# Optimization experiments

Hardware: AMD Instinct MI355X
Metric: run time of the kernel (lower is better)

Reference implementation:

```python
import jax, jax.numpy as jnp
import numpy as np

D = 1024
H = 16
HD = D // H
N_TEXT = 256
N_VISION = 256
N_FRAMES = 12


def setup_inputs() -> dict:
    key = jax.random.key(0)
    ks = jax.random.split(key, 10)
    s = 1.0 / np.sqrt(D)
    return {
        "text_hidden_states": jax.random.normal(ks[0], (N_TEXT, D), jnp.float32),
        "vision_hidden_states": jax.random.normal(ks[1], (N_VISION, N_FRAMES, D), jnp.float32),
        "wq": jax.random.normal(ks[2], (D, D), jnp.float32) * s,
        "bq": jnp.zeros((D,), jnp.float32),
        "wk": jax.random.normal(ks[3], (D, D), jnp.float32) * s,
        "bk": jnp.zeros((D,), jnp.float32),
        "wv": jax.random.normal(ks[4], (D, D), jnp.float32) * s,
        "bv": jnp.zeros((D,), jnp.float32),
        "wo": jax.random.normal(ks[5], (D, D), jnp.float32) * s,
        "bo": jnp.zeros((D,), jnp.float32),
    }


def reference(text_hidden_states, vision_hidden_states, wq, bq, wk, bk, wv, bv, wo, bo):
    n_text = text_hidden_states.shape[0]
    n_vision, n_frames, _ = vision_hidden_states.shape
    # projections (torch Linear: x @ W.T + b)
    q = (text_hidden_states @ wq.T + bq).reshape(n_text, H, HD)            # [t,h,d]
    k = (vision_hidden_states @ wk.T + bk).reshape(n_vision, n_frames, H, HD)  # [v,f,h,d]
    v = (vision_hidden_states @ wv.T + bv).reshape(n_vision, n_frames, H, HD)  # [v,f,h,d]
    # shared query broadcast over vision batch: scores [v,h,f,t]
    scores = jnp.einsum("vfhd,thd->vhft", k, q) / jnp.sqrt(jnp.asarray(HD, scores_dtype := q.dtype))
    probs = jax.nn.softmax(scores, axis=2)  # softmax over frames (dim=2)
    # attn_output [v,t,h,d] -> [v,t,D]
    out = jnp.einsum("vfhd,vhft->vthd", v, probs).reshape(n_vision, n_text, D)
    return out @ wo.T + bo
```

## Files before the change

### kernel.cpp

```cpp
#include <hip/hip_runtime.h>

typedef short bf16x8 __attribute__((ext_vector_type(8)));
typedef float f32x4 __attribute__((ext_vector_type(4)));

__device__ __forceinline__ unsigned short f2bf(float f) {
  union { float f; unsigned u; } x; x.f = f;
  unsigned u = x.u;
  u += 0x7fffu + ((u >> 16) & 1u);
  return (unsigned short)(u >> 16);
}

__global__ __launch_bounds__(256) void cvt_all(
    const float* __restrict__ text, const float* __restrict__ vis,
    const float* __restrict__ wq, const float* __restrict__ wk,
    const float* __restrict__ wv, const float* __restrict__ wo,
    unsigned short* __restrict__ o0, unsigned short* __restrict__ o1,
    unsigned short* __restrict__ o2, unsigned short* __restrict__ o3,
    unsigned short* __restrict__ o4, unsigned short* __restrict__ o5)
{
  long i4 = (long)blockIdx.x * 256 + threadIdx.x;
  const float* src; unsigned short* dst; long base;
  if      (i4 <   65536) { src = text; dst = o0; base = 0; }
  else if (i4 <  851968) { src = vis;  dst = o1; base = 65536; }
  else if (i4 < 1114112) { src = wq;   dst = o2; base = 851968; }
  else if (i4 < 1376256) { src = wk;   dst = o3; base = 1114112; }
  else if (i4 < 1638400) { src = wv;   dst = o4; base = 1376256; }
  else                   { src = wo;   dst = o5; base = 1638400; }
  long li = i4 - base;
  float4 f = reinterpret_cast<const float4*>(src)[li];
  uint2 u;
  u.x = (unsigned)f2bf(f.x) | ((unsigned)f2bf(f.y) << 16);
  u.y = (unsigned)f2bf(f.z) | ((unsigned)f2bf(f.w) << 16);
  reinterpret_cast<uint2*>(dst)[li] = u;
}

__global__ __launch_bounds__(256) void gemm_abt_bf16(
    const unsigned short* __restrict__ A,
    const unsigned short* __restrict__ B,
    unsigned short* __restrict__ C,
    const float* __restrict__ bias,
    int K, int lda, int ldb, int ldc)
{
  __shared__ unsigned short As[64][40];
  __shared__ unsigned short Bs[64][40];
  const int m0 = blockIdx.y * 64, n0 = blockIdx.x * 64;
  const int tid = threadIdx.x;
  const int lane = tid & 63, w = tid >> 6;
  const int wm = w >> 1, wn = w & 1;
  const int r16 = lane & 15, kg = lane >> 4;
  const int srow = tid >> 2, sseg = tid & 3;

  const f32x4 fzero = {0.f, 0.f, 0.f, 0.f};
  f32x4 acc[2][2];
#pragma unroll
  for (int i = 0; i < 2; ++i)
#pragma unroll
    for (int j = 0; j < 2; ++j) acc[i][j] = fzero;

  for (int k0 = 0; k0 < K; k0 += 32) {
    __syncthreads();
    *reinterpret_cast<int4*>(&As[srow][sseg * 8]) =
        *reinterpret_cast<const int4*>(&A[(long)(m0 + srow) * lda + k0 + sseg * 8]);
    *reinterpret_cast<int4*>(&Bs[srow][sseg * 8]) =
        *reinterpret_cast<const int4*>(&B[(long)(n0 + srow) * ldb + k0 + sseg * 8]);
    __syncthreads();
    bf16x8 a[2], b[2];
#pragma unroll
    for (int i = 0; i < 2; ++i)
      a[i] = *reinterpret_cast<const bf16x8*>(&As[wm * 32 + i * 16 + r16][kg * 8]);
#pragma unroll
    for (int j = 0; j < 2; ++j)
      b[j] = *reinterpret_cast<const bf16x8*>(&Bs[wn * 32 + j * 16 + r16][kg * 8]);
#pragma unroll
    for (int i = 0; i < 2; ++i)
#pragma unroll
      for (int j = 0; j < 2; ++j)
        acc[i][j] = __builtin_amdgcn_mfma_f32_16x16x32_bf16(a[i], b[j], acc[i][j], 0, 0, 0);
  }
#pragma unroll
  for (int i = 0; i < 2; ++i) {
#pragma unroll
    for (int j = 0; j < 2; ++j) {
      const int row = m0 + wm * 32 + i * 16 + kg * 4;
      const int col = n0 + wn * 32 + j * 16 + r16;
      const float bv = bias ? bias[col] : 0.f;
#pragma unroll
      for (int r = 0; r < 4; ++r)
        C[(long)(row + r) * ldc + col] = f2bf(acc[i][j][r] + bv);
    }
  }
}

__global__ __launch_bounds__(256) void gemm_abt_bf16_kv(
    const unsigned short* __restrict__ A,
    const unsigned short* __restrict__ B0,
    const unsigned short* __restrict__ B1,
    unsigned short* __restrict__ C0,
    unsigned short* __restrict__ C1,
    const float* __restrict__ bias0,
    const float* __restrict__ bias1,
    int K, int lda, int ldb, int ldc)
{
  const unsigned short* B = blockIdx.z ? B1 : B0;
  unsigned short* C = blockIdx.z ? C1 : C0;
  const float* bias = blockIdx.z ? bias1 : bias0;

  __shared__ unsigned short As[64][40];
  __shared__ unsigned short Bs[64][40];
  const int m0 = blockIdx.y * 64, n0 = blockIdx.x * 64;
  const int tid = threadIdx.x;
  const int lane = tid & 63, w = tid >> 6;
  const int wm = w >> 1, wn = w & 1;
  const int r16 = lane & 15, kg = lane >> 4;
  const int srow = tid >> 2, sseg = tid & 3;

  const f32x4 fzero = {0.f, 0.f, 0.f, 0.f};
  f32x4 acc[2][2];
#pragma unroll
  for (int i = 0; i < 2; ++i)
#pragma unroll
    for (int j = 0; j < 2; ++j) acc[i][j] = fzero;

  for (int k0 = 0; k0 < K; k0 += 32) {
    __syncthreads();
    *reinterpret_cast<int4*>(&As[srow][sseg * 8]) =
        *reinterpret_cast<const int4*>(&A[(long)(m0 + srow) * lda + k0 + sseg * 8]);
    *reinterpret_cast<int4*>(&Bs[srow][sseg * 8]) =
        *reinterpret_cast<const int4*>(&B[(long)(n0 + srow) * ldb + k0 + sseg * 8]);
    __syncthreads();
    bf16x8 a[2], b[2];
#pragma unroll
    for (int i = 0; i < 2; ++i)
      a[i] = *reinterpret_cast<const bf16x8*>(&As[wm * 32 + i * 16 + r16][kg * 8]);
#pragma unroll
    for (int j = 0; j < 2; ++j)
      b[j] = *reinterpret_cast<const bf16x8*>(&Bs[wn * 32 + j * 16 + r16][kg * 8]);
#pragma unroll
    for (int i = 0; i < 2; ++i)
#pragma unroll
      for (int j = 0; j < 2; ++j)
        acc[i][j] = __builtin_amdgcn_mfma_f32_16x16x32_bf16(a[i], b[j], acc[i][j], 0, 0, 0);
  }
#pragma unroll
  for (int i = 0; i < 2; ++i) {
#pragma unroll
    for (int j = 0; j < 2; ++j) {
      const int row = m0 + wm * 32 + i * 16 + kg * 4;
      const int col = n0 + wn * 32 + j * 16 + r16;
      const float bv = bias ? bias[col] : 0.f;
#pragma unroll
      for (int r = 0; r < 4; ++r)
        C[(long)(row + r) * ldc + col] = f2bf(acc[i][j][r] + bv);
    }
  }
}

__global__ __launch_bounds__(256) void scores_softmax(
    const unsigned short* __restrict__ Kp,
    const unsigned short* __restrict__ Qp,
    unsigned short* __restrict__ P)
{
  const int h = blockIdx.x, v = blockIdx.y;
  const int tid = threadIdx.x, lane = tid & 63, w = tid >> 6;
  const int r16 = lane & 15, kg = lane >> 4;
  __shared__ unsigned short Ks[16][72];
  __shared__ unsigned short Qs[256][72];

  if (tid < 96) {
    const int f = tid >> 3, seg = tid & 7;
    *reinterpret_cast<int4*>(&Ks[f][seg * 8]) =
        *reinterpret_cast<const int4*>(&Kp[(long)(v * 12 + f) * 1024 + h * 64 + seg * 8]);
  } else if (tid < 128) {
    const int f = 12 + ((tid - 96) >> 3), seg = (tid - 96) & 7;
    int4 z; z.x = 0; z.y = 0; z.z = 0; z.w = 0;
    *reinterpret_cast<int4*>(&Ks[f][seg * 8]) = z;
  }
#pragma unroll
  for (int rep = 0; rep < 8; ++rep) {
    const int row = rep * 32 + (tid >> 3), seg = tid & 7;
    *reinterpret_cast<int4*>(&Qs[row][seg * 8]) =
        *reinterpret_cast<const int4*>(&Qp[(long)row * 1024 + h * 64 + seg * 8]);
  }
  __syncthreads();

  const f32x4 fzero = {0.f, 0.f, 0.f, 0.f};
  f32x4 acc[4];
#pragma unroll
  for (int j = 0; j < 4; ++j) acc[j] = fzero;

#pragma unroll
  for (int kk = 0; kk < 64; kk += 32) {
    bf16x8 a = *reinterpret_cast<const bf16x8*>(&Ks[r16][kk + kg * 8]);
#pragma unroll
    for (int j = 0; j < 4; ++j) {
      bf16x8 b = *reinterpret_cast<const bf16x8*>(&Qs[w * 64 + j * 16 + r16][kk + kg * 8]);
      acc[j] = __builtin_amdgcn_mfma_f32_16x16x32_bf16(a, b, acc[j], 0, 0, 0);
    }
  }
#pragma unroll
  for (int j = 0; j < 4; ++j) {
    float lm = -1e30f;
    if (kg < 3) {
#pragma unroll
      for (int r = 0; r < 4; ++r) lm = fmaxf(lm, acc[j][r] * 0.125f);
    }
    lm = fmaxf(lm, __shfl_xor(lm, 16));
    lm = fmaxf(lm, __shfl_xor(lm, 32));
    float p[4]; float ls = 0.f;
    if (kg < 3) {
#pragma unroll
      for (int r = 0; r < 4; ++r) { p[r] = __expf(acc[j][r] * 0.125f - lm); ls += p[r]; }
    }
    ls += __shfl_xor(ls, 16);
    ls += __shfl_xor(ls, 32);
    const float inv = 1.f / ls;
    if (kg < 3) {
      const int t = w * 64 + j * 16 + r16;
      uint2 u2;
      u2.x = (unsigned)f2bf(p[0] * inv) | ((unsigned)f2bf(p[1] * inv) << 16);
      u2.y = (unsigned)f2bf(p[2] * inv) | ((unsigned)f2bf(p[3] * inv) << 16);
      *reinterpret_cast<uint2*>(&P[((long)v * 256 + t) * 192 + h * 12 + kg * 4]) = u2;
    }
  }
}

__global__ __launch_bounds__(256) void combine(
    const unsigned short* __restrict__ VPp,
    const unsigned short* __restrict__ Wo,
    const unsigned short* __restrict__ P,
    const float* __restrict__ bo,
    float* __restrict__ out)
{
  const int wgid = blockIdx.x;
  const int xcd = wgid & 7, idx = wgid >> 3;
  const int v = ((idx & 31) << 3) | xcd;
  const int n0 = (idx >> 5) << 6;

  const int tid = threadIdx.x, lane = tid & 63, w = tid >> 6;
  const int r16 = lane & 15, kg = lane >> 4;

  __shared__ unsigned short BsAll[64 * 192];

  const unsigned short* VPv = VPp + (long)v * 12 * 1024;
#pragma unroll
  for (int hi = 0; hi < 4; ++hi) {
    const int h = (w << 2) + hi;
    const int db = h * 64;
    f32x4 accp[4] = {{0.f,0.f,0.f,0.f},{0.f,0.f,0.f,0.f},{0.f,0.f,0.f,0.f},{0.f,0.f,0.f,0.f}};
#pragma unroll
    for (int kk = 0; kk < 64; kk += 32) {
      bf16x8 a = {0,0,0,0,0,0,0,0};
      if (r16 < 12)
        a = *reinterpret_cast<const bf16x8*>(&VPv[(long)r16 * 1024 + db + kk + kg * 8]);
      bf16x8 bfr[4];
#pragma unroll
      for (int j = 0; j < 4; ++j)
        bfr[j] = *reinterpret_cast<const bf16x8*>(
            &Wo[(long)(n0 + j * 16 + r16) * 1024 + db + kk + kg * 8]);
#pragma unroll
      for (int j = 0; j < 4; ++j)
        accp[j] = __builtin_amdgcn_mfma_f32_16x16x32_bf16(a, bfr[j], accp[j], 0, 0, 0);
    }
    if (kg < 3) {
      const int k = h * 12 + kg * 4;
#pragma unroll
      for (int j = 0; j < 4; ++j) {
        const int o = j * 16 + r16;
        uint2 u2;
        u2.x = (unsigned)f2bf(accp[j][0]) | ((unsigned)f2bf(accp[j][1]) << 16);
        u2.y = (unsigned)f2bf(accp[j][2]) | ((unsigned)f2bf(accp[j][3]) << 16);
        *reinterpret_cast<uint2*>(
            &BsAll[o * 192 + (((k >> 3) ^ (o & 7)) << 3) + (k & 7)]) = u2;
      }
    }
  }

  const unsigned short* Pv = P + (long)v * 256 * 192;
  bf16x8 pB[2][4];
#pragma unroll
  for (int s = 0; s < 2; ++s)
#pragma unroll
    for (int i = 0; i < 4; ++i)
      pB[s][i] = *reinterpret_cast<const bf16x8*>(
          &Pv[(long)(w * 64 + i * 16 + r16) * 192 + s * 32 + kg * 8]);

  f32x4 bias4[4];
#pragma unroll
  for (int j = 0; j < 4; ++j)
    bias4[j] = *reinterpret_cast<const f32x4*>(&bo[n0 + j * 16 + kg * 4]);

  __syncthreads();

  f32x4 acc[4][4];
#pragma unroll
  for (int j = 0; j < 4; ++j)
#pragma unroll
    for (int i = 0; i < 4; ++i) { f32x4 z = {0.f,0.f,0.f,0.f}; acc[j][i] = z; }

#pragma unroll
  for (int s = 0; s < 6; ++s) {
    const int k0 = s * 32;
    bf16x8 zA[4];
#pragma unroll
    for (int j = 0; j < 4; ++j) {
      const int row = j * 16 + r16;
      const int slot = (k0 >> 3) + kg;
      zA[j] = *reinterpret_cast<const bf16x8*>(
          &BsAll[row * 192 + ((slot ^ (row & 7)) << 3)]);
    }
    bf16x8 pC[4];
#pragma unroll
    for (int i = 0; i < 4; ++i) pC[i] = pB[s & 1][i];
    if (s < 4) {
#pragma unroll
      for (int i = 0; i < 4; ++i)
        pB[s & 1][i] = *reinterpret_cast<const bf16x8*>(
            &Pv[(long)(w * 64 + i * 16 + r16) * 192 + (k0 + 64) + kg * 8]);
    }
#pragma unroll
    for (int j = 0; j < 4; ++j)
#pragma unroll
      for (int i = 0; i < 4; ++i)
        acc[j][i] = __builtin_amdgcn_mfma_f32_16x16x32_bf16(zA[j], pC[i], acc[j][i], 0, 0, 0);
  }

  float* outv = out + (long)v * 256 * 1024;
#pragma unroll
  for (int i = 0; i < 4; ++i) {
    const long tbase = (long)(w * 64 + i * 16 + r16) * 1024;
#pragma unroll
    for (int j = 0; j < 4; ++j) {
      f32x4 vle = acc[j][i] + bias4[j];
      *reinterpret_cast<f32x4*>(&outv[tbase + n0 + j * 16 + kg * 4]) = vle;
    }
  }
}

extern "C" void kernel_launch(void* const* d_in, const int* in_sizes, int n_in,
                              void* d_out, int out_size, void* d_ws, size_t ws_size,
                              hipStream_t stream) {
  const float* text = (const float*)d_in[0];
  const float* vis  = (const float*)d_in[1];
  const float* wq   = (const float*)d_in[2];
  const float* bq   = (const float*)d_in[3];
  const float* wk   = (const float*)d_in[4];
  const float* bk   = (const float*)d_in[5];
  const float* wv   = (const float*)d_in[6];
  const float* bv   = (const float*)d_in[7];
  const float* wo   = (const float*)d_in[8];
  const float* bo   = (const float*)d_in[9];
  float* out = (float*)d_out;

  unsigned short* text16 = (unsigned short*)d_ws;
  unsigned short* vis16  = text16 + 262144;
  unsigned short* wq16   = vis16  + 3145728;
  unsigned short* wk16   = wq16   + 1048576;
  unsigned short* wv16   = wk16   + 1048576;
  unsigned short* wo16   = wv16   + 1048576;
  unsigned short* q16    = wo16   + 1048576;
  unsigned short* k16    = q16    + 262144;
  unsigned short* vp16   = k16    + 3145728;
  unsigned short* P      = vp16   + 3145728;

  cvt_all<<<7424, 256, 0, stream>>>(text, vis, wq, wk, wv, wo,
                                    text16, vis16, wq16, wk16, wv16, wo16);
  gemm_abt_bf16<<<dim3(16, 4), 256, 0, stream>>>(text16, wq16, q16, bq, 1024, 1024, 1024, 1024);
  gemm_abt_bf16_kv<<<dim3(16, 48, 2), 256, 0, stream>>>(
      vis16, wk16, wv16, k16, vp16, bk, bv, 1024, 1024, 1024, 1024);
  scores_softmax<<<dim3(16, 256), 256, 0, stream>>>(k16, q16, P);
  combine<<<4096, 256, 0, stream>>>(vp16, wo16, P, bo, out);
}
```

Before: 232.9 us.

## Split combine into Z-precompute kernel and separate output GEMM with chunked workspace

Splits the fused combine kernel in two. The first kernel computes the per-vision Z = VP·Wo^T fragments and writes them to a global workspace buffer. The second kernel does the output GEMM against P, tiling over text rows and reading Z from global memory. Both run in v-chunks sized to the available workspace. This changes the tiling so the output GEMM can use a different work split and register reuse, at the cost of an extra round trip of Z (about 50MB for the full chunk) through global memory and extra kernel launches.

```diff
diff --git a/kernel.cpp b/kernel.cpp
--- a/kernel.cpp
+++ b/kernel.cpp
@@ -224,17 +224,17 @@
   }
 }
 
-__global__ __launch_bounds__(256) void combine(
+__global__ __launch_bounds__(256) void zh_kernel(
     const unsigned short* __restrict__ VPp,
     const unsigned short* __restrict__ Wo,
-    const unsigned short* __restrict__ P,
-    const float* __restrict__ bo,
-    float* __restrict__ out)
+    unsigned short* __restrict__ Z,
+    int vbase, int vsh)
 {
   const int wgid = blockIdx.x;
   const int xcd = wgid & 7, idx = wgid >> 3;
-  const int v = ((idx & 31) << 3) | xcd;
-  const int n0 = (idx >> 5) << 6;
+  const int vlocal = ((idx & ((1 << vsh) - 1)) << 3) | xcd;
+  const int v = vbase + vlocal;
+  const int n0 = (idx >> vsh) << 6;
 
   const int tid = threadIdx.x, lane = tid & 63, w = tid >> 6;
   const int r16 = lane & 15, kg = lane >> 4;
@@ -274,65 +274,70 @@
       }
     }
   }
-
-  const unsigned short* Pv = P + (long)v * 256 * 192;
-  bf16x8 pB[2][4];
-#pragma unroll
-  for (int s = 0; s < 2; ++s)
-#pragma unroll
-    for (int i = 0; i < 4; ++i)
-      pB[s][i] = *reinterpret_cast<const bf16x8*>(
-          &Pv[(long)(w * 64 + i * 16 + r16) * 192 + s * 32 + kg * 8]);
-
-  f32x4 bias4[4];
-#pragma unroll
-  for (int j = 0; j < 4; ++j)
-    bias4[j] = *reinterpret_cast<const f32x4*>(&bo[n0 + j * 16 + kg * 4]);
-
   __syncthreads();
-
-  f32x4 acc[4][4];
-#pragma unroll
-  for (int j = 0; j < 4; ++j)
-#pragma unroll
-    for (int i = 0; i < 4; ++i) { f32x4 z = {0.f,0.f,0.f,0.f}; acc[j][i] = z; }
-
-#pragma unroll
-  for (int s = 0; s < 6; ++s) {
-    const int k0 = s * 32;
-    bf16x8 zA[4];
-#pragma unroll
-    for (int j = 0; j < 4; ++j) {
-      const int row = j * 16 + r16;
-      const int slot = (k0 >> 3) + kg;
-      zA[j] = *reinterpret_cast<const bf16x8*>(
-          &BsAll[row * 192 + ((slot ^ (row & 7)) << 3)]);
-    }
-    bf16x8 pC[4];
-#pragma unroll
-    for (int i = 0; i < 4; ++i) pC[i] = pB[s & 1][i];
-    if (s < 4) {
-#pragma unroll
-      for (int i = 0; i < 4; ++i)
-        pB[s & 1][i] = *reinterpret_cast<const bf16x8*>(
-            &Pv[(long)(w * 64 + i * 16 + r16) * 192 + (k0 + 64) + kg * 8]);
-    }
-#pragma unroll
-    for (int j = 0; j < 4; ++j)
-#pragma unroll
-      for (int i = 0; i < 4; ++i)
-        acc[j][i] = __builtin_amdgcn_mfma_f32_16x16x32_bf16(zA[j], pC[i], acc[j][i], 0, 0, 0);
-  }
-
-  float* outv = out + (long)v * 256 * 1024;
-#pragma unroll
-  for (int i = 0; i < 4; ++i) {
-    const long tbase = (long)(w * 64 + i * 16 + r16) * 1024;
-#pragma unroll
-    for (int j = 0; j < 4; ++j) {
-      f32x4 vle = acc[j][i] + bias4[j];
-      *reinterpret_cast<f32x4*>(&outv[tbase + n0 + j * 16 + kg * 4]) = vle;
-    }
+  unsigned short* Zv = Z + ((long)vlocal * 1024 + n0) * 192;
+  const int row = tid >> 2;
+#pragma unroll
+  for (int rep = 0; rep < 6; ++rep) {
+    const int slot = (tid & 3) + (rep << 2);
+    *reinterpret_cast<int4*>(&Zv[(long)row * 192 + slot * 8]) =
+        *reinterpret_cast<const int4*>(&BsAll[row * 192 + ((slot ^ (row & 7)) << 3)]);
+  }
+}
+
+__global__ __launch_bounds__(256) void out_gemm2(
+    const unsigned short* __restrict__ Z,
+    const unsigned short* __restrict__ P,
+    const float* __restrict__ bo,
+    float* __restrict__ out,
+    int vbase, int vsh)
+{
+  const int wgid = blockIdx.x;
+  const int xcd = wgid & 7, idx = wgid >> 3;
+  const int vlocal = ((idx & ((1 << vsh) - 1)) << 3) | xcd;
+  const int v = vbase + vlocal;
+  const int t0 = (idx >> vsh) << 4;
+
+  const int tid = threadIdx.x, lane = tid & 63, w = tid >> 6;
+  const int r16 = lane & 15, kg = lane >> 4;
+
+  const unsigned short* Pv = P + ((long)v * 256 + t0) * 192;
+  bf16x8 pf[6];
+#pragma unroll
+  for (int s = 0; s < 6; ++s)
+    pf[s] = *reinterpret_cast<const bf16x8*>(&Pv[(long)r16 * 192 + s * 32 + kg * 8]);
+
+  const unsigned short* Zw = Z + ((long)vlocal * 1024 + w * 256) * 192;
+  const float* bow = bo + w * 256 + kg * 4;
+  float* outw = out + ((long)v * 256 + t0 + r16) * 1024 + w * 256 + kg * 4;
+
+  bf16x8 zf[3][6];
+  f32x4 bb[3];
+#pragma unroll
+  for (int d = 0; d < 3; ++d) {
+#pragma unroll
+    for (int s = 0; s < 6; ++s)
+      zf[d][s] = *reinterpret_cast<const bf16x8*>(
+          &Zw[(long)(d * 16 + r16) * 192 + s * 32 + kg * 8]);
+    bb[d] = *reinterpret_cast<const f32x4*>(&bow[d * 16]);
+  }
+
+#pragma unroll
+  for (int j = 0; j < 16; ++j) {
+    const int d = j % 3;
+    f32x4 acc = {0.f, 0.f, 0.f, 0.f};
+#pragma unroll
+    for (int s = 0; s < 6; ++s)
+      acc = __builtin_amdgcn_mfma_f32_16x16x32_bf16(zf[d][s], pf[s], acc, 0, 0, 0);
+    acc += bb[d];
+    if (j < 13) {
+#pragma unroll
+      for (int s = 0; s < 6; ++s)
+        zf[d][s] = *reinterpret_cast<const bf16x8*>(
+            &Zw[(long)((j + 3) * 16 + r16) * 192 + s * 32 + kg * 8]);
+      bb[d] = *reinterpret_cast<const f32x4*>(&bow[(j + 3) * 16]);
+    }
+    *reinterpret_cast<f32x4*>(&outw[j * 16]) = acc;
   }
 }
 
@@ -361,6 +366,13 @@
   unsigned short* k16    = q16    + 262144;
   unsigned short* vp16   = k16    + 3145728;
   unsigned short* P      = vp16   + 3145728;
+  unsigned short* Zbuf   = P     + 12582912;
+  const size_t base_shorts = 26738688;
+
+  size_t avail_shorts = (ws_size / 2 > base_shorts) ? (ws_size / 2 - base_shorts) : 0;
+  int vchunk = 256;
+  while (vchunk > 8 && (size_t)vchunk * 1024 * 192 > avail_shorts) vchunk >>= 1;
+  int vsh = 0; { int t = vchunk >> 3; while (t > 1) { t >>= 1; ++vsh; } }
 
   cvt_all<<<7424, 256, 0, stream>>>(text, vis, wq, wk, wv, wo,
                                     text16, vis16, wq16, wk16, wv16, wo16);
@@ -368,5 +380,8 @@
   gemm_abt_bf16_kv<<<dim3(16, 48, 2), 256, 0, stream>>>(
       vis16, wk16, wv16, k16, vp16, bk, bv, 1024, 1024, 1024, 1024);
   scores_softmax<<<dim3(16, 256), 256, 0, stream>>>(k16, q16, P);
-  combine<<<4096, 256, 0, stream>>>(vp16, wo16, P, bo, out);
-}
+  for (int vb = 0; vb < 256; vb += vchunk) {
+    zh_kernel<<<16 * vchunk, 256, 0, stream>>>(vp16, wo16, Zbuf, vb, vsh);
+    out_gemm2<<<16 * vchunk, 256, 0, stream>>>(Zbuf, P, bo, out, vb, vsh);
+  }
+}
```

New measurement: 436.6 us. 1.87x slower.

## Use 128x128 GEMM tiles with direct global-to-LDS loads for projections

Applied to the files above, without the earlier changes.

Replaces the 64x64-tile projection GEMMs with a single 128x128-tile kernel in which each wave computes a 64x64 sub-tile as a 4x4 grid of MFMAs. Operand tiles are staged with global_load_lds (direct global-to-LDS DMA) instead of passing through registers. The larger tile cuts global and LDS traffic per MFMA and raises arithmetic intensity. In exchange, the Q projection runs on only 16 blocks, and the unpadded LDS layout may cause bank conflicts on fragment reads.

```diff
diff --git a/kernel.cpp b/kernel.cpp
--- a/kernel.cpp
+++ b/kernel.cpp
@@ -2,6 +2,8 @@
 
 typedef short bf16x8 __attribute__((ext_vector_type(8)));
 typedef float f32x4 __attribute__((ext_vector_type(4)));
+typedef const unsigned int __attribute__((address_space(1)))* gas1;
+typedef unsigned int __attribute__((address_space(3)))* las3;
 
 __device__ __forceinline__ unsigned short f2bf(float f) {
   union { float f; unsigned u; } x; x.f = f;
@@ -34,64 +36,7 @@
   reinterpret_cast<uint2*>(dst)[li] = u;
 }
 
-__global__ __launch_bounds__(256) void gemm_abt_bf16(
-    const unsigned short* __restrict__ A,
-    const unsigned short* __restrict__ B,
-    unsigned short* __restrict__ C,
-    const float* __restrict__ bias,
-    int K, int lda, int ldb, int ldc)
-{
-  __shared__ unsigned short As[64][40];
-  __shared__ unsigned short Bs[64][40];
-  const int m0 = blockIdx.y * 64, n0 = blockIdx.x * 64;
-  const int tid = threadIdx.x;
-  const int lane = tid & 63, w = tid >> 6;
-  const int wm = w >> 1, wn = w & 1;
-  const int r16 = lane & 15, kg = lane >> 4;
-  const int srow = tid >> 2, sseg = tid & 3;
-
-  const f32x4 fzero = {0.f, 0.f, 0.f, 0.f};
-  f32x4 acc[2][2];
-#pragma unroll
-  for (int i = 0; i < 2; ++i)
-#pragma unroll
-    for (int j = 0; j < 2; ++j) acc[i][j] = fzero;
-
-  for (int k0 = 0; k0 < K; k0 += 32) {
-    __syncthreads();
-    *reinterpret_cast<int4*>(&As[srow][sseg * 8]) =
-        *reinterpret_cast<const int4*>(&A[(long)(m0 + srow) * lda + k0 + sseg * 8]);
-    *reinterpret_cast<int4*>(&Bs[srow][sseg * 8]) =
-        *reinterpret_cast<const int4*>(&B[(long)(n0 + srow) * ldb + k0 + sseg * 8]);
-    __syncthreads();
-    bf16x8 a[2], b[2];
-#pragma unroll
-    for (int i = 0; i < 2; ++i)
-      a[i] = *reinterpret_cast<const bf16x8*>(&As[wm * 32 + i * 16 + r16][kg * 8]);
-#pragma unroll
-    for (int j = 0; j < 2; ++j)
-      b[j] = *reinterpret_cast<const bf16x8*>(&Bs[wn * 32 + j * 16 + r16][kg * 8]);
-#pragma unroll
-    for (int i = 0; i < 2; ++i)
-#pragma unroll
-      for (int j = 0; j < 2; ++j)
-        acc[i][j] = __builtin_amdgcn_mfma_f32_16x16x32_bf16(a[i], b[j], acc[i][j], 0, 0, 0);
-  }
-#pragma unroll
-  for (int i = 0; i < 2; ++i) {
-#pragma unroll
-    for (int j = 0; j < 2; ++j) {
-      const int row = m0 + wm * 32 + i * 16 + kg * 4;
-      const int col = n0 + wn * 32 + j * 16 + r16;
-      const float bv = bias ? bias[col] : 0.f;
-#pragma unroll
-      for (int r = 0; r < 4; ++r)
-        C[(long)(row + r) * ldc + col] = f2bf(acc[i][j][r] + bv);
-    }
-  }
-}
-
-__global__ __launch_bounds__(256) void gemm_abt_bf16_kv(
+__global__ __launch_bounds__(256) void gemm128(
     const unsigned short* __restrict__ A,
     const unsigned short* __restrict__ B0,
     const unsigned short* __restrict__ B1,
@@ -105,48 +50,55 @@
   unsigned short* C = blockIdx.z ? C1 : C0;
   const float* bias = blockIdx.z ? bias1 : bias0;
 
-  __shared__ unsigned short As[64][40];
-  __shared__ unsigned short Bs[64][40];
-  const int m0 = blockIdx.y * 64, n0 = blockIdx.x * 64;
+  __shared__ unsigned short As[128 * 32];
+  __shared__ unsigned short Bs[128 * 32];
+  const int m0 = blockIdx.y * 128, n0 = blockIdx.x * 128;
   const int tid = threadIdx.x;
   const int lane = tid & 63, w = tid >> 6;
-  const int wm = w >> 1, wn = w & 1;
+  const int wr = w >> 1, wc = w & 1;
   const int r16 = lane & 15, kg = lane >> 4;
-  const int srow = tid >> 2, sseg = tid & 3;
-
-  const f32x4 fzero = {0.f, 0.f, 0.f, 0.f};
-  f32x4 acc[2][2];
-#pragma unroll
-  for (int i = 0; i < 2; ++i)
-#pragma unroll
-    for (int j = 0; j < 2; ++j) acc[i][j] = fzero;
+  const int lrow = lane >> 2, lseg = lane & 3;
+
+  f32x4 acc[4][4];
+#pragma unroll
+  for (int i = 0; i < 4; ++i)
+#pragma unroll
+    for (int j = 0; j < 4; ++j) { f32x4 z = {0.f,0.f,0.f,0.f}; acc[i][j] = z; }
 
   for (int k0 = 0; k0 < K; k0 += 32) {
     __syncthreads();
-    *reinterpret_cast<int4*>(&As[srow][sseg * 8]) =
-        *reinterpret_cast<const int4*>(&A[(long)(m0 + srow) * lda + k0 + sseg * 8]);
-    *reinterpret_cast<int4*>(&Bs[srow][sseg * 8]) =
-        *reinterpret_cast<const int4*>(&B[(long)(n0 + srow) * ldb + k0 + sseg * 8]);
+#pragma unroll
+    for (int i = 0; i < 2; ++i) {
+      const int c = w * 2 + i;
+      __builtin_amdgcn_global_load_lds(
+          (gas1)(const void*)&A[(long)(m0 + c * 16 + lrow) * lda + k0 + lseg * 8],
+          (las3)(void*)&As[c * 512], 16, 0, 0);
+      __builtin_amdgcn_global_load_lds(
+          (gas1)(const void*)&B[(long)(n0 + c * 16 + lrow) * ldb + k0 + lseg * 8],
+          (las3)(void*)&Bs[c * 512], 16, 0, 0);
+    }
     __syncthreads();
-    bf16x8 a[2], b[2];
-#pragma unroll
-    for (int i = 0; i < 2; ++i)
-      a[i] = *reinterpret_cast<const bf16x8*>(&As[wm * 32 + i * 16 + r16][kg * 8]);
-#pragma unroll
-    for (int j = 0; j < 2; ++j)
-      b[j] = *reinterpret_cast<const bf16x8*>(&Bs[wn * 32 + j * 16 + r16][kg * 8]);
-#pragma unroll
-    for (int i = 0; i < 2; ++i)
-#pragma unroll
-      for (int j = 0; j < 2; ++j)
+
+    bf16x8 a[4], b[4];
+#pragma unroll
+    for (int i = 0; i < 4; ++i)
+      a[i] = *reinterpret_cast<const bf16x8*>(&As[(wr * 64 + i * 16 + r16) * 32 + kg * 8]);
+#pragma unroll
+    for (int j = 0; j < 4; ++j)
+      b[j] = *reinterpret_cast<const bf16x8*>(&Bs[(wc * 64 + j * 16 + r16) * 32 + kg * 8]);
+#pragma unroll
+    for (int i = 0; i < 4; ++i)
+#pragma unroll
+      for (int j = 0; j < 4; ++j)
         acc[i][j] = __builtin_amdgcn_mfma_f32_16x16x32_bf16(a[i], b[j], acc[i][j], 0, 0, 0);
   }
-#pragma unroll
-  for (int i = 0; i < 2; ++i) {
-#pragma unroll
-    for (int j = 0; j < 2; ++j) {
-      const int row = m0 + wm * 32 + i * 16 + kg * 4;
-      const int col = n0 + wn * 32 + j * 16 + r16;
+
+#pragma unroll
+  for (int i = 0; i < 4; ++i) {
+#pragma unroll
+    for (int j = 0; j < 4; ++j) {
+      const int row = m0 + wr * 64 + i * 16 + kg * 4;
+      const int col = n0 + wc * 64 + j * 16 + r16;
       const float bv = bias ? bias[col] : 0.f;
 #pragma unroll
       for (int r = 0; r < 4; ++r)
@@ -364,8 +316,9 @@
 
   cvt_all<<<7424, 256, 0, stream>>>(text, vis, wq, wk, wv, wo,
                                     text16, vis16, wq16, wk16, wv16, wo16);
-  gemm_abt_bf16<<<dim3(16, 4), 256, 0, stream>>>(text16, wq16, q16, bq, 1024, 1024, 1024, 1024);
-  gemm_abt_bf16_kv<<<dim3(16, 48, 2), 256, 0, stream>>>(
+  gemm128<<<dim3(8, 2, 1), 256, 0, stream>>>(
+      text16, wq16, wq16, q16, q16, bq, bq, 1024, 1024, 1024, 1024);
+  gemm128<<<dim3(8, 24, 2), 256, 0, stream>>>(
       vis16, wk16, wv16, k16, vp16, bk, bv, 1024, 1024, 1024, 1024);
   scores_softmax<<<dim3(16, 256), 256, 0, stream>>>(k16, q16, P);
   combine<<<4096, 256, 0, stream>>>(vp16, wo16, P, bo, out);
```

New measurement: 242.9 us. 4.3% more time.
